# Performance work log

Hardware: AMD Instinct MI355X
Metric: run time of the kernel (lower is better)

## Reference

```python
import jax, jax.numpy as jnp
import numpy as np

B = 65536
IN = 64
H = 128
OUT = 2


def setup_inputs() -> dict:
    key = jax.random.key(0)
    ks = jax.random.split(key, 16)
    s_in = 1.0 / np.sqrt(IN)
    s_h = 1.0 / np.sqrt(H)
    d = {}
    d["x"] = jax.random.normal(ks[0], (B, IN), dtype=jnp.float32)
    # initial state (module resets to zeros per day)
    d["h0"] = jnp.zeros((H,), dtype=jnp.float32)
    d["c0"] = jnp.zeros((B, H), dtype=jnp.float32)
    # input->hidden linears (with bias), torch Linear layout [out, in]
    for i, name in enumerate(["f", "i", "o", "c"]):
        d[f"Wx{name}"] = jax.random.uniform(ks[1 + i], (H, IN), jnp.float32, -s_in, s_in)
        d[f"bx{name}"] = jax.random.uniform(ks[5 + i], (H,), jnp.float32, -s_in, s_in)
        d[f"Wh{name}"] = jax.random.uniform(ks[9 + i], (H, H), jnp.float32, -s_h, s_h)
    d["Wy"] = jax.random.uniform(ks[13], (OUT, H), jnp.float32, -s_h, s_h)
    d["by"] = jax.random.uniform(ks[14], (OUT,), jnp.float32, -s_h, s_h)
    return d


def reference(x, h0, c0, Wxf, bxf, Wxi, bxi, Wxo, bxo, Wxc, bxc, Whf, Whi, Who, Whc, Wy, by):
    # hidden recurrent contributions (h0 is a length-H vector, broadcast over batch)
    hi = h0 @ Whi.T  # [H]
    hf = h0 @ Whf.T
    ho = h0 @ Who.T
    hc = h0 @ Whc.T
    i = jax.nn.sigmoid(x @ Wxi.T + bxi + hi)  # [B, H]
    f = jax.nn.sigmoid(x @ Wxf.T + bxf + hf)
    o = jax.nn.sigmoid(x @ Wxo.T + bxo + ho)
    c_til = jnp.tanh(x @ Wxc.T + bxc + hc)
    c = f * c0 + i * c_til
    h = o * jnp.tanh(c)
    y_hat = h @ Wy.T + by  # [B, OUT]
    return y_hat
```

## Files before the change

kernel.cpp:

```cpp
#include <hip/hip_runtime.h>


#define B_SIZE 65536

typedef __bf16 bf16x8 __attribute__((ext_vector_type(8)));
typedef __bf16 bf16x4 __attribute__((ext_vector_type(4)));
typedef float f32x4 __attribute__((ext_vector_type(4)));

__device__ __forceinline__ float fsig(float x) {
    float e = __builtin_amdgcn_exp2f(-1.442695040888963f * x);
    return __builtin_amdgcn_rcpf(1.0f + e);
}
__device__ __forceinline__ float ftanh(float x) {
    float e = __builtin_amdgcn_exp2f(2.885390081777927f * x);
    return 1.0f - 2.0f * __builtin_amdgcn_rcpf(e + 1.0f);
}

__global__ void bias_kernel(const float* __restrict__ h0,
                            const float* __restrict__ Whf, const float* __restrict__ Whi,
                            const float* __restrict__ Who, const float* __restrict__ Whc,
                            const float* __restrict__ bxf, const float* __restrict__ bxi,
                            const float* __restrict__ bxo, const float* __restrict__ bxc,
                            float* __restrict__ bias512) {
    int j = blockIdx.x * 64 + threadIdx.x;
    int g = j >> 7, r = j & 127;
    const float* Wh = (g == 0) ? Whf : (g == 1) ? Whi : (g == 2) ? Who : Whc;
    const float* bx = (g == 0) ? bxf : (g == 1) ? bxi : (g == 2) ? bxo : bxc;
    float s = bx[r];
    const float* row = Wh + r * 128;
#pragma unroll 8
    for (int k = 0; k < 128; ++k) s += h0[k] * row[k];
    bias512[j] = s;
}

__launch_bounds__(256, 2)
__global__ void lstm_kernel(const float* __restrict__ x, const float* __restrict__ c0,
                            const float* __restrict__ Wxf, const float* __restrict__ Wxi,
                            const float* __restrict__ Wxo, const float* __restrict__ Wxc,
                            const float* __restrict__ Wy, const float* __restrict__ by,
                            const float* __restrict__ bias512, float* __restrict__ out) {
    __shared__ __bf16 xs[1024];
    __shared__ float yred[4][16][2];

    const int tid  = threadIdx.x;
    const int lane = tid & 63;
    const int w    = tid >> 6;
    const int q    = lane >> 4;
    const int n15  = lane & 15;

    const float* Wxg[4] = {Wxf, Wxi, Wxo, Wxc};
    bf16x8 bw[4][2][2];
    float biasv[4][2];
#pragma unroll
    for (int g = 0; g < 4; ++g) {
#pragma unroll
        for (int cb = 0; cb < 2; ++cb) {
            const int n = w * 32 + cb * 16 + n15;
            biasv[g][cb] = bias512[g * 128 + n];
#pragma unroll
            for (int kb = 0; kb < 2; ++kb) {
                const float* p = Wxg[g] + n * 64 + kb * 32 + q * 8;
                float4 lo = *(const float4*)p;
                float4 hi = *(const float4*)(p + 4);
                bf16x8 v;
                v[0] = (__bf16)lo.x; v[1] = (__bf16)lo.y; v[2] = (__bf16)lo.z; v[3] = (__bf16)lo.w;
                v[4] = (__bf16)hi.x; v[5] = (__bf16)hi.y; v[6] = (__bf16)hi.z; v[7] = (__bf16)hi.w;
                bw[g][cb][kb] = v;
            }
        }
    }
    float wyv[2][2];
#pragma unroll
    for (int o = 0; o < 2; ++o)
#pragma unroll
        for (int cb = 0; cb < 2; ++cb)
            wyv[o][cb] = Wy[o * 128 + w * 32 + cb * 16 + n15];
    const float by0 = by[0], by1 = by[1];

    constexpr int ITERS = (B_SIZE / 16) / 512;
    const int tile0 = blockIdx.x * ITERS;

    const int xrow = tid >> 4;
    const int k4   = (tid & 15) * 4;
    const int sidx = (k4 >> 5) * 512 + ((k4 & 31) >> 3) * 128 + xrow * 8 + (k4 & 7);

    float4 xr = *(const float4*)(x + (size_t)(tile0 * 16 + xrow) * 64 + k4);
    {
        bf16x4 v; v[0] = (__bf16)xr.x; v[1] = (__bf16)xr.y; v[2] = (__bf16)xr.z; v[3] = (__bf16)xr.w;
        *(bf16x4*)&xs[sidx] = v;
    }
    __syncthreads();

    for (int it = 0; it < ITERS; ++it) {
        const int tile = tile0 + it;
        const int b0 = tile * 16;

        bf16x8 a0 = *(const bf16x8*)&xs[lane * 8];
        bf16x8 a1 = *(const bf16x8*)&xs[512 + lane * 8];

        const int tn = (it + 1 < ITERS) ? (tile + 1) : tile;
        xr = *(const float4*)(x + (size_t)(tn * 16 + xrow) * 64 + k4);

        float c0v[2][4];
#pragma unroll
        for (int cb = 0; cb < 2; ++cb)
#pragma unroll
            for (int r = 0; r < 4; ++r)
                c0v[cb][r] = c0[(size_t)(b0 + q * 4 + r) * 128 + w * 32 + cb * 16 + n15];

        f32x4 acc[4][2];
#pragma unroll
        for (int g = 0; g < 4; ++g)
#pragma unroll
            for (int cb = 0; cb < 2; ++cb) {
                float b = biasv[g][cb];
                f32x4 t = {b, b, b, b};
                acc[g][cb] = t;
            }
#pragma unroll
        for (int g = 0; g < 4; ++g)
#pragma unroll
            for (int cb = 0; cb < 2; ++cb) {
                acc[g][cb] = __builtin_amdgcn_mfma_f32_16x16x32_bf16(a0, bw[g][cb][0], acc[g][cb], 0, 0, 0);
                acc[g][cb] = __builtin_amdgcn_mfma_f32_16x16x32_bf16(a1, bw[g][cb][1], acc[g][cb], 0, 0, 0);
            }

        float p0[4] = {0.f, 0.f, 0.f, 0.f};
        float p1[4] = {0.f, 0.f, 0.f, 0.f};
#pragma unroll
        for (int cb = 0; cb < 2; ++cb)
#pragma unroll
            for (int r = 0; r < 4; ++r) {
                float fg = fsig(acc[0][cb][r]);
                float ig = fsig(acc[1][cb][r]);
                float og = fsig(acc[2][cb][r]);
                float ct = ftanh(acc[3][cb][r]);
                float c  = fg * c0v[cb][r] + ig * ct;
                float h  = og * ftanh(c);
                p0[r] += h * wyv[0][cb];
                p1[r] += h * wyv[1][cb];
            }
#pragma unroll
        for (int m = 1; m < 16; m <<= 1) {
#pragma unroll
            for (int r = 0; r < 4; ++r) {
                p0[r] += __shfl_xor(p0[r], m, 64);
                p1[r] += __shfl_xor(p1[r], m, 64);
            }
        }
        if (n15 == 0) {
#pragma unroll
            for (int r = 0; r < 4; ++r) {
                yred[w][q * 4 + r][0] = p0[r];
                yred[w][q * 4 + r][1] = p1[r];
            }
        }
        __syncthreads();
        if (tid < 32) {
            int row = tid >> 1, o = tid & 1;
            float s = (o ? by1 : by0) + yred[0][row][o] + yred[1][row][o] +
                      yred[2][row][o] + yred[3][row][o];
            out[(size_t)(b0 + row) * 2 + o] = s;
        }
        {
            bf16x4 v; v[0] = (__bf16)xr.x; v[1] = (__bf16)xr.y; v[2] = (__bf16)xr.z; v[3] = (__bf16)xr.w;
            *(bf16x4*)&xs[sidx] = v;
        }
        __syncthreads();
    }
}

extern "C" void kernel_launch(void* const* d_in, const int* in_sizes, int n_in,
                              void* d_out, int out_size, void* d_ws, size_t ws_size,
                              hipStream_t stream) {
    const float* x   = (const float*)d_in[0];
    const float* h0  = (const float*)d_in[1];
    const float* c0  = (const float*)d_in[2];
    const float* Wxf = (const float*)d_in[3];
    const float* bxf = (const float*)d_in[4];
    const float* Whf = (const float*)d_in[5];
    const float* Wxi = (const float*)d_in[6];
    const float* bxi = (const float*)d_in[7];
    const float* Whi = (const float*)d_in[8];
    const float* Wxo = (const float*)d_in[9];
    const float* bxo = (const float*)d_in[10];
    const float* Who = (const float*)d_in[11];
    const float* Wxc = (const float*)d_in[12];
    const float* bxc = (const float*)d_in[13];
    const float* Whc = (const float*)d_in[14];
    const float* Wy  = (const float*)d_in[15];
    const float* by  = (const float*)d_in[16];
    float* out = (float*)d_out;
    float* bias512 = (float*)d_ws;

    bias_kernel<<<8, 64, 0, stream>>>(h0, Whf, Whi, Who, Whc, bxf, bxi, bxo, bxc, bias512);
    lstm_kernel<<<512, 256, 0, stream>>>(x, c0, Wxf, Wxi, Wxo, Wxc, Wy, by, bias512, out);
}
```

Measured before the change: 135.7 us.

## Prefetch c0 tiles through LDS and double the grid size

Result: slower. 163.0 us (+20.1%).

```diff
diff --git a/kernel.cpp b/kernel.cpp
--- a/kernel.cpp
+++ b/kernel.cpp
@@ -27,19 +27,24 @@
     const float* Wh = (g == 0) ? Whf : (g == 1) ? Whi : (g == 2) ? Who : Whc;
     const float* bx = (g == 0) ? bxf : (g == 1) ? bxi : (g == 2) ? bxo : bxc;
     float s = bx[r];
-    const float* row = Wh + r * 128;
+    const float4* row = (const float4*)(Wh + r * 128);
+    const float4* h4  = (const float4*)h0;
 #pragma unroll 8
-    for (int k = 0; k < 128; ++k) s += h0[k] * row[k];
+    for (int k = 0; k < 32; ++k) {
+        float4 a = row[k], b = h4[k];
+        s += a.x * b.x + a.y * b.y + a.z * b.z + a.w * b.w;
+    }
     bias512[j] = s;
 }
 
-__launch_bounds__(256, 2)
+__launch_bounds__(256, 4)
 __global__ void lstm_kernel(const float* __restrict__ x, const float* __restrict__ c0,
                             const float* __restrict__ Wxf, const float* __restrict__ Wxi,
                             const float* __restrict__ Wxo, const float* __restrict__ Wxc,
                             const float* __restrict__ Wy, const float* __restrict__ by,
                             const float* __restrict__ bias512, float* __restrict__ out) {
     __shared__ __bf16 xs[1024];
+    __shared__ float cs[16 * 132];
     __shared__ float yred[4][16][2];
 
     const int tid  = threadIdx.x;
@@ -77,17 +82,24 @@
             wyv[o][cb] = Wy[o * 128 + w * 32 + cb * 16 + n15];
     const float by0 = by[0], by1 = by[1];
 
-    constexpr int ITERS = (B_SIZE / 16) / 512;
+    constexpr int ITERS = (B_SIZE / 16) / 1024;
     const int tile0 = blockIdx.x * ITERS;
 
     const int xrow = tid >> 4;
     const int k4   = (tid & 15) * 4;
     const int sidx = (k4 >> 5) * 512 + ((k4 & 31) >> 3) * 128 + xrow * 8 + (k4 & 7);
 
+    const int ccol = (tid & 15) * 8;
+    const int cidx = xrow * 132 + ccol;
+
     float4 xr = *(const float4*)(x + (size_t)(tile0 * 16 + xrow) * 64 + k4);
+    float4 cpa = *(const float4*)(c0 + (size_t)(tile0 * 16 + xrow) * 128 + ccol);
+    float4 cpb = *(const float4*)(c0 + (size_t)(tile0 * 16 + xrow) * 128 + ccol + 4);
     {
         bf16x4 v; v[0] = (__bf16)xr.x; v[1] = (__bf16)xr.y; v[2] = (__bf16)xr.z; v[3] = (__bf16)xr.w;
         *(bf16x4*)&xs[sidx] = v;
+        *(float4*)&cs[cidx] = cpa;
+        *(float4*)&cs[cidx + 4] = cpb;
     }
     __syncthreads();
 
@@ -98,15 +110,17 @@
         bf16x8 a0 = *(const bf16x8*)&xs[lane * 8];
         bf16x8 a1 = *(const bf16x8*)&xs[512 + lane * 8];
 
+        float c0v[2][4];
+#pragma unroll
+        for (int cb = 0; cb < 2; ++cb)
+#pragma unroll
+            for (int r = 0; r < 4; ++r)
+                c0v[cb][r] = cs[(q * 4 + r) * 132 + w * 32 + cb * 16 + n15];
+
         const int tn = (it + 1 < ITERS) ? (tile + 1) : tile;
-        xr = *(const float4*)(x + (size_t)(tn * 16 + xrow) * 64 + k4);
-
-        float c0v[2][4];
-#pragma unroll
-        for (int cb = 0; cb < 2; ++cb)
-#pragma unroll
-            for (int r = 0; r < 4; ++r)
-                c0v[cb][r] = c0[(size_t)(b0 + q * 4 + r) * 128 + w * 32 + cb * 16 + n15];
+        xr  = *(const float4*)(x  + (size_t)(tn * 16 + xrow) * 64 + k4);
+        cpa = *(const float4*)(c0 + (size_t)(tn * 16 + xrow) * 128 + ccol);
+        cpb = *(const float4*)(c0 + (size_t)(tn * 16 + xrow) * 128 + ccol + 4);
 
         f32x4 acc[4][2];
 #pragma unroll
@@ -156,15 +170,18 @@
             }
         }
         __syncthreads();
-        if (tid < 32) {
-            int row = tid >> 1, o = tid & 1;
-            float s = (o ? by1 : by0) + yred[0][row][o] + yred[1][row][o] +
-                      yred[2][row][o] + yred[3][row][o];
-            out[(size_t)(b0 + row) * 2 + o] = s;
+        if (tid < 16) {
+            int row = tid;
+            float s0 = by0 + yred[0][row][0] + yred[1][row][0] + yred[2][row][0] + yred[3][row][0];
+            float s1 = by1 + yred[0][row][1] + yred[1][row][1] + yred[2][row][1] + yred[3][row][1];
+            float2 s = {s0, s1};
+            *(float2*)(out + (size_t)(b0 + row) * 2) = s;
         }
         {
             bf16x4 v; v[0] = (__bf16)xr.x; v[1] = (__bf16)xr.y; v[2] = (__bf16)xr.z; v[3] = (__bf16)xr.w;
             *(bf16x4*)&xs[sidx] = v;
+            *(float4*)&cs[cidx] = cpa;
+            *(float4*)&cs[cidx + 4] = cpb;
         }
         __syncthreads();
     }
@@ -194,5 +211,5 @@
     float* bias512 = (float*)d_ws;
 
     bias_kernel<<<8, 64, 0, stream>>>(h0, Whf, Whi, Who, Whc, bxf, bxi, bxo, bxc, bias512);
-    lstm_kernel<<<512, 256, 0, stream>>>(x, c0, Wxf, Wxi, Wxo, Wxc, Wy, by, bias512, out);
-}
+    lstm_kernel<<<1024, 256, 0, stream>>>(x, c0, Wxf, Wxi, Wxo, Wxc, Wy, by, bias512, out);
+}
```
